# Kernel tuning notes

Hardware: AMD Instinct MI355X
Metric: run time of the kernel (lower is better)

The kernel has to match this reference:

```python
import jax, jax.numpy as jnp
import numpy as np

N_HEAD = 16


def setup_inputs() -> dict:
    key = jax.random.key(0)
    ks = jax.random.split(key, 5)
    B, L, C = 2, 2048, 1024
    s = 0.02
    return {
        "x": jax.random.normal(ks[0], (B, L, C), dtype=jnp.float32),
        "attn_mask": jnp.ones((B, L), dtype=jnp.int64),
        "Wq": jax.random.normal(ks[1], (C, C), dtype=jnp.float32) * s,
        "Wk": jax.random.normal(ks[2], (C, C), dtype=jnp.float32) * s,
        "Wv": jax.random.normal(ks[3], (C, C), dtype=jnp.float32) * s,
        "Wp": jax.random.normal(ks[4], (C, C), dtype=jnp.float32) * s,
    }


def reference(x, attn_mask, Wq, Wk, Wv, Wp):
    B, L, C = x.shape
    H = N_HEAD
    D = C // H
    # nn.Linear(bias=False): y = x @ W.T with W of shape (out, in)
    q = (x @ Wq.T).reshape(B, L, H, D).transpose(0, 2, 1, 3)  # (B,H,L,D)
    k = (x @ Wk.T).reshape(B, L, H, D).transpose(0, 2, 1, 3)
    v = (x @ Wv.T).reshape(B, L, H, D).transpose(0, 2, 1, 3)
    att = jnp.einsum("bhqd,bhkd->bhqk", q, k) / jnp.sqrt(jnp.asarray(D, x.dtype))
    causal = jnp.tril(jnp.ones((L, L), dtype=bool))  # (L,L)
    tok = (attn_mask != 0)[:, None, None, :]  # (B,1,1,L) key-side padding mask
    mask = causal[None, None, :, :] & tok
    att = jnp.where(mask, att, -jnp.inf)
    att = jax.nn.softmax(att, axis=-1)
    # dropout p=0.0 (eval): identity
    y = jnp.einsum("bhqk,bhkd->bhqd", att, v)
    y = y.transpose(0, 2, 1, 3).reshape(B, L, C)
    return y @ Wp.T
```

## Files before the change

### kernel.cpp

```cpp
#include <hip/hip_runtime.h>
#include <hip/hip_bf16.h>
#include <cstdint>

typedef _Float16 f16;
typedef _Float16 f16x4 __attribute__((ext_vector_type(4)));
typedef _Float16 f16x8 __attribute__((ext_vector_type(8)));
typedef float f32x4 __attribute__((ext_vector_type(4)));

#define LNEG (-1e30f)
#define EXP2(x) __builtin_amdgcn_exp2f(x)

__device__ __forceinline__ f32x4 mfma16(f16x8 a, f16x8 b, f32x4 c){
    return __builtin_amdgcn_mfma_f32_16x16x32_f16(a, b, c, 0, 0, 0);
}

__global__ __launch_bounds__(256) void cvt5(
    const float* __restrict__ x,  const float* __restrict__ wq,
    const float* __restrict__ wk, const float* __restrict__ wv,
    const float* __restrict__ wp, f16* __restrict__ dst, int nx4, int nw4)
{
    int i = blockIdx.x * blockDim.x + threadIdx.x;
    const float* src; int off;
    if (i < nx4){ src = x; off = i; }
    else {
        int j = i - nx4;
        int s = j >> 18;
        off = j & (nw4 - 1);
        src = (s == 0) ? wq : (s == 1) ? wk : (s == 2) ? wv : wp;
    }
    float4 v = ((const float4*)src)[off];
    f16x4 o = { (f16)v.x, (f16)v.y, (f16)v.z, (f16)v.w };
    *(f16x4*)&dst[(size_t)i * 4] = o;
}

template<typename OutT>
__global__ __launch_bounds__(256) void gemm_xwt(
    const f16* __restrict__ A, const f16* __restrict__ W0, size_t wstride,
    OutT* __restrict__ out0, size_t ostride, f16* __restrict__ vtout,
    int M, int N, int K)
{
    const int tid  = threadIdx.x;
    const int lane = tid & 63;
    const int w    = tid >> 6;
    const int wr   = w >> 1, wc = w & 1;
    const int m0   = blockIdx.y * 128;
    const int n0   = blockIdx.x * 128;
    const f16* Wz  = W0 + wstride * blockIdx.z;
    OutT* out      = out0 + ostride * blockIdx.z;

    __shared__ f16 At[2][128 * 64];
    __shared__ f16 Bt[2][128 * 64];

    f32x4 acc[4][4] = {};
    f16x8 avr[4], bvr[4];

    int srow[4], scolb[4], sswz[4];
    #pragma unroll
    for (int j = 0; j < 4; ++j){
        int off  = (j * 256 + tid) * 16;
        srow[j]  = off >> 7;
        scolb[j] = off & 127;
        sswz[j]  = srow[j] * 128 + (scolb[j] ^ ((srow[j] & 7) << 4));
    }

    #pragma unroll
    for (int j = 0; j < 4; ++j){
        avr[j] = *(const f16x8*)&A [(size_t)(m0 + srow[j]) * K + (scolb[j] >> 1)];
        bvr[j] = *(const f16x8*)&Wz[(size_t)(n0 + srow[j]) * K + (scolb[j] >> 1)];
    }
    #pragma unroll
    for (int j = 0; j < 4; ++j){
        *(f16x8*)((char*)At[0] + sswz[j]) = avr[j];
        *(f16x8*)((char*)Bt[0] + sswz[j]) = bvr[j];
    }
    __syncthreads();

    const int NT = K >> 6;
    for (int t = 0; t < NT; ++t){
        const int cur = t & 1;
        const bool pre = (t + 1 < NT);
        if (pre){
            const int k0 = (t + 1) << 6;
            #pragma unroll
            for (int j = 0; j < 4; ++j){
                avr[j] = *(const f16x8*)&A [(size_t)(m0 + srow[j]) * K + k0 + (scolb[j] >> 1)];
                bvr[j] = *(const f16x8*)&Wz[(size_t)(n0 + srow[j]) * K + k0 + (scolb[j] >> 1)];
            }
        }
        #pragma unroll
        for (int kk = 0; kk < 2; ++kk){
            f16x8 af[4], bf[4];
            #pragma unroll
            for (int mf = 0; mf < 4; ++mf){
                int row = wr * 64 + mf * 16 + (lane & 15);
                int cb  = (kk * 64 + 16 * (lane >> 4)) ^ ((row & 7) << 4);
                af[mf] = *(const f16x8*)((const char*)At[cur] + row * 128 + cb);
            }
            #pragma unroll
            for (int nf = 0; nf < 4; ++nf){
                int row = wc * 64 + nf * 16 + (lane & 15);
                int cb  = (kk * 64 + 16 * (lane >> 4)) ^ ((row & 7) << 4);
                bf[nf] = *(const f16x8*)((const char*)Bt[cur] + row * 128 + cb);
            }
            #pragma unroll
            for (int mf = 0; mf < 4; ++mf)
                #pragma unroll
                for (int nf = 0; nf < 4; ++nf)
                    acc[mf][nf] = mfma16(af[mf], bf[nf], acc[mf][nf]);
        }
        if (pre){
            const int nb = cur ^ 1;
            #pragma unroll
            for (int j = 0; j < 4; ++j){
                *(f16x8*)((char*)At[nb] + sswz[j]) = avr[j];
                *(f16x8*)((char*)Bt[nb] + sswz[j]) = bvr[j];
            }
        }
        __syncthreads();
    }

    if (vtout != nullptr && blockIdx.z == 2){
        #pragma unroll
        for (int mf = 0; mf < 4; ++mf)
            #pragma unroll
            for (int nf = 0; nf < 4; ++nf){
                int row = m0 + wr * 64 + mf * 16 + 4 * (lane >> 4);
                int col = n0 + wc * 64 + nf * 16 + (lane & 15);
                int bb = row >> 11, ll = row & 2047;
                int bh = bb * 16 + (col >> 6), dd = col & 63;
                f16x4 o = { (f16)acc[mf][nf][0], (f16)acc[mf][nf][1],
                            (f16)acc[mf][nf][2], (f16)acc[mf][nf][3] };
                *(f16x4*)&vtout[((size_t)(bh * 64 + dd)) * 2048 + ll] = o;
            }
    } else {
        #pragma unroll
        for (int mf = 0; mf < 4; ++mf)
            #pragma unroll
            for (int nf = 0; nf < 4; ++nf)
                #pragma unroll
                for (int r = 0; r < 4; ++r){
                    int row = m0 + wr * 64 + mf * 16 + 4 * (lane >> 4) + r;
                    int col = n0 + wc * 64 + nf * 16 + (lane & 15);
                    out[(size_t)row * N + col] = (OutT)acc[mf][nf][r];
                }
    }
}

__global__ __launch_bounds__(256, 4) void attn_fused(
    const f16* __restrict__ q, const f16* __restrict__ k,
    const f16* __restrict__ vt, const int* __restrict__ amask,
    f16* __restrict__ y)
{
    const int tid  = threadIdx.x;
    const int lane = tid & 63;
    const int w    = tid >> 6;
    const int g    = lane >> 4;
    const int qq   = lane & 15;

    const int lin = blockIdx.x;
    const int bh  = ((lin & 7) << 2) | ((lin >> 3) & 3);
    const int qtv = (lin >> 5) & 31;
    const int q5  = (qtv & 7) | ((qtv & 16) >> 1);
    const int qt  = (qtv & 8) ? (31 - q5) : q5;
    const int b = bh >> 4, h = bh & 15;
    const int q0w = qt * 64 + w * 16;
    const int nkt = qt + 1;

    __shared__ char sK[2][64 * 128];
    __shared__ char sV[2][64 * 128];
    __shared__ char sP[4][16 * 128];

    const int srow = (tid * 2) >> 3;
    const int sc8a = (tid * 2) & 7, sc8b = sc8a + 1;
    const int swka = (sc8a * 16) ^ ((srow & 7) << 4);
    const int swkb = (sc8b * 16) ^ ((srow & 7) << 4);
    const f16* kbase  = k  + ((size_t)b * 2048) * 1024 + h * 64;
    const f16* vtbase = vt + (size_t)bh * 64 * 2048;

    const f16 qscale = (f16)(0.125f * 1.44269504088896f);
    f16x8 aq[2];
    #pragma unroll
    for (int f = 0; f < 2; ++f){
        aq[f] = *(const f16x8*)&q[((size_t)(b * 2048 + q0w + qq)) * 1024 + h * 64 + f * 32 + 8 * g];
        #pragma unroll
        for (int j = 0; j < 8; ++j) aq[f][j] *= qscale;
    }

    f32x4 acc_o[4] = {};
    float m_ln = LNEG, l_ln = 0.f;

    char* pbase = sP[w] + qq * 128;
    const int swp = (qq & 7) << 4;

    {
        f16x8 ka  = *(const f16x8*)(kbase  + (size_t)srow * 1024 + sc8a * 8);
        f16x8 kb2 = *(const f16x8*)(kbase  + (size_t)srow * 1024 + sc8b * 8);
        f16x8 va  = *(const f16x8*)(vtbase + (size_t)srow * 2048 + sc8a * 8);
        f16x8 vb  = *(const f16x8*)(vtbase + (size_t)srow * 2048 + sc8b * 8);
        *(f16x8*)(sK[0] + srow * 128 + swka) = ka;
        *(f16x8*)(sK[0] + srow * 128 + swkb) = kb2;
        *(f16x8*)(sV[0] + srow * 128 + swka) = va;
        *(f16x8*)(sV[0] + srow * 128 + swkb) = vb;
    }
    __syncthreads();

    for (int kt = 0; kt < nkt; ++kt){
        const int cur = kt & 1;
        const int k0 = kt * 64;
        const bool pre = (kt + 1 < nkt);

        f16x8 ka, kb2, va, vb;
        if (pre){
            const int nk0 = k0 + 64;
            ka  = *(const f16x8*)(kbase  + (size_t)(nk0 + srow) * 1024 + sc8a * 8);
            kb2 = *(const f16x8*)(kbase  + (size_t)(nk0 + srow) * 1024 + sc8b * 8);
            va  = *(const f16x8*)(vtbase + (size_t)srow * 2048 + nk0 + sc8a * 8);
            vb  = *(const f16x8*)(vtbase + (size_t)srow * 2048 + nk0 + sc8b * 8);
        }

        unsigned long long tokbits = __ballot(amask[b * 2048 + k0 + lane] != 0);
        const bool tokall = (tokbits == ~0ull);

        f32x4 acc_s[4] = {};
        #pragma unroll
        for (int kf = 0; kf < 4; ++kf){
            const int keyl = kf * 16 + qq;
            const char* kr = sK[cur] + keyl * 128;
            const int sw = (keyl & 7) << 4;
            #pragma unroll
            for (int f = 0; f < 2; ++f){
                f16x8 ak = *(const f16x8*)(kr + ((f * 64 + 16 * g) ^ sw));
                acc_s[kf] = mfma16(ak, aq[f], acc_s[kf]);
            }
        }

        const bool fullt = (k0 + 63 <= q0w) && tokall;
        float sv[16];
        #pragma unroll
        for (int kf = 0; kf < 4; ++kf)
            #pragma unroll
            for (int r = 0; r < 4; ++r){
                float s = acc_s[kf][r];
                if (!fullt){
                    const int keyl = kf * 16 + 4 * g + r;
                    const bool ok = (k0 + keyl <= q0w + qq) && ((tokbits >> keyl) & 1);
                    s = ok ? s : LNEG;
                }
                sv[kf * 4 + r] = s;
            }

        float tmax = sv[0];
        #pragma unroll
        for (int i = 1; i < 16; ++i) tmax = fmaxf(tmax, sv[i]);
        tmax = fmaxf(tmax, __shfl_xor(tmax, 16));
        tmax = fmaxf(tmax, __shfl_xor(tmax, 32));
        const bool skip = __all(tmax <= m_ln + 8.f);
        float alpha = 1.f;
        if (!skip){
            const float newm = fmaxf(m_ln, tmax);
            alpha = EXP2(m_ln - newm);
            m_ln = newm;
        }
        float rs = 0.f;
        #pragma unroll
        for (int i = 0; i < 16; ++i){ sv[i] = EXP2(sv[i] - m_ln); rs += sv[i]; }
        rs += __shfl_xor(rs, 16);
        rs += __shfl_xor(rs, 32);
        l_ln = l_ln * alpha + rs;
        if (!skip){
            #pragma unroll
            for (int r = 0; r < 4; ++r){
                const float ar = __shfl(alpha, 4 * g + r);
                #pragma unroll
                for (int nf = 0; nf < 4; ++nf) acc_o[nf][r] *= ar;
            }
        }

        #pragma unroll
        for (int kf = 0; kf < 4; ++kf){
            f16x4 pk = { (f16)sv[kf*4+0], (f16)sv[kf*4+1], (f16)sv[kf*4+2], (f16)sv[kf*4+3] };
            *(f16x4*)(pbase + ((kf * 32 + 8 * g) ^ swp)) = pk;
        }
        __builtin_amdgcn_wave_barrier();

        #pragma unroll
        for (int f = 0; f < 2; ++f){
            f16x8 ap = *(const f16x8*)(pbase + ((f * 64 + 16 * g) ^ swp));
            #pragma unroll
            for (int nf = 0; nf < 4; ++nf){
                const int d = nf * 16 + qq;
                f16x8 bv = *(const f16x8*)(sV[cur] + d * 128 + ((f * 64 + 16 * g) ^ ((d & 7) << 4)));
                acc_o[nf] = mfma16(ap, bv, acc_o[nf]);
            }
        }
        __builtin_amdgcn_wave_barrier();

        if (pre){
            const int nb = cur ^ 1;
            *(f16x8*)(sK[nb] + srow * 128 + swka) = ka;
            *(f16x8*)(sK[nb] + srow * 128 + swkb) = kb2;
            *(f16x8*)(sV[nb] + srow * 128 + swka) = va;
            *(f16x8*)(sV[nb] + srow * 128 + swkb) = vb;
        }
        __syncthreads();
    }

    const float invl = 1.f / l_ln;
    #pragma unroll
    for (int r = 0; r < 4; ++r){
        const float ir = __shfl(invl, 4 * g + r);
        const int row = q0w + 4 * g + r;
        #pragma unroll
        for (int nf = 0; nf < 4; ++nf)
            y[((size_t)(b * 2048 + row)) * 1024 + h * 64 + nf * 16 + qq] = (f16)(acc_o[nf][r] * ir);
    }
}

extern "C" void kernel_launch(void* const* d_in, const int* in_sizes, int n_in,
                              void* d_out, int out_size, void* d_ws, size_t ws_size,
                              hipStream_t stream){
    const float* x  = (const float*)d_in[0];
    const int*   am = (const int*)d_in[1];
    const float* Wq = (const float*)d_in[2];
    const float* Wk = (const float*)d_in[3];
    const float* Wv = (const float*)d_in[4];
    const float* Wp = (const float*)d_in[5];
    float* out = (float*)d_out;

    char* ws = (char*)d_ws;
    const size_t XE = (size_t)4096 * 1024;
    const size_t WE = (size_t)1024 * 1024;

    f16* x16 = (f16*)(ws);
    f16* w16 = (f16*)(ws + XE * 2);
    f16* qkv = (f16*)(ws + XE * 2 + WE * 8);
    f16* vt  = (f16*)(ws + XE * 2 + WE * 8 + XE * 6);
    f16* y16 = (f16*)(ws + XE * 2 + WE * 8 + XE * 8);

    cvt5<<<8192, 256, 0, stream>>>(x, Wq, Wk, Wv, Wp, x16,
                                   (int)(XE / 4), (int)(WE / 4));

    gemm_xwt<f16><<<dim3(8, 32, 3), 256, 0, stream>>>(x16, w16, WE, qkv, XE, vt, 4096, 1024, 1024);

    attn_fused<<<dim3(1024), 256, 0, stream>>>(qkv, qkv + XE, vt, am, y16);

    gemm_xwt<float><<<dim3(8, 32, 1), 256, 0, stream>>>(y16, w16 + 3 * WE, 0, out, 0, nullptr, 4096, 1024, 1024);
}
```

Baseline: 114.1 us.

## Software-pipeline QK^T of next tile with softmax/PV of current tile

Restructures the flash-attention key loop so the QK^T MFMAs for tile kt+1 are issued before the softmax and PV work of tile kt, and global prefetch now runs two tiles ahead. The intent is to overlap matrix-core work with the scalar softmax and LDS traffic, and to hide global-load latency behind more work. In exchange it holds an extra set of score accumulators in registers, which may lower occupancy. It also adds a second block-wide barrier per iteration around the shared-memory refill.

```diff
diff --git a/kernel.cpp b/kernel.cpp
--- a/kernel.cpp
+++ b/kernel.cpp
@@ -204,46 +204,82 @@
     }
     __syncthreads();
 
+    f32x4 accA[4] = {};
+    unsigned long long tok_cur;
+    {
+        const bool has1 = (nkt > 1);
+        f16x8 ka, kb2, va, vb;
+        if (has1){
+            ka  = *(const f16x8*)(kbase  + (size_t)(64 + srow) * 1024 + sc8a * 8);
+            kb2 = *(const f16x8*)(kbase  + (size_t)(64 + srow) * 1024 + sc8b * 8);
+            va  = *(const f16x8*)(vtbase + (size_t)srow * 2048 + 64 + sc8a * 8);
+            vb  = *(const f16x8*)(vtbase + (size_t)srow * 2048 + 64 + sc8b * 8);
+        }
+        const int amv0 = amask[b * 2048 + lane];
+        #pragma unroll
+        for (int kf = 0; kf < 4; ++kf){
+            const int keyl = kf * 16 + qq;
+            const char* kr = sK[0] + keyl * 128;
+            const int sw = (keyl & 7) << 4;
+            #pragma unroll
+            for (int f = 0; f < 2; ++f){
+                f16x8 ak = *(const f16x8*)(kr + ((f * 64 + 16 * g) ^ sw));
+                accA[kf] = mfma16(ak, aq[f], accA[kf]);
+            }
+        }
+        tok_cur = __ballot(amv0 != 0);
+        if (has1){
+            *(f16x8*)(sK[1] + srow * 128 + swka) = ka;
+            *(f16x8*)(sK[1] + srow * 128 + swkb) = kb2;
+            *(f16x8*)(sV[1] + srow * 128 + swka) = va;
+            *(f16x8*)(sV[1] + srow * 128 + swkb) = vb;
+        }
+    }
+    __syncthreads();
+
     for (int kt = 0; kt < nkt; ++kt){
-        const int cur = kt & 1;
+        const int cur = kt & 1, nb = cur ^ 1;
         const int k0 = kt * 64;
-        const bool pre = (kt + 1 < nkt);
+        const bool has1 = (kt + 1 < nkt);
+        const bool has2 = (kt + 2 < nkt);
 
         f16x8 ka, kb2, va, vb;
-        if (pre){
-            const int nk0 = k0 + 64;
+        int amv;
+        if (has2){
+            const int nk0 = k0 + 128;
             ka  = *(const f16x8*)(kbase  + (size_t)(nk0 + srow) * 1024 + sc8a * 8);
             kb2 = *(const f16x8*)(kbase  + (size_t)(nk0 + srow) * 1024 + sc8b * 8);
             va  = *(const f16x8*)(vtbase + (size_t)srow * 2048 + nk0 + sc8a * 8);
             vb  = *(const f16x8*)(vtbase + (size_t)srow * 2048 + nk0 + sc8b * 8);
         }
-
-        unsigned long long tokbits = __ballot(amask[b * 2048 + k0 + lane] != 0);
-        const bool tokall = (tokbits == ~0ull);
-
-        f32x4 acc_s[4] = {};
-        #pragma unroll
-        for (int kf = 0; kf < 4; ++kf){
-            const int keyl = kf * 16 + qq;
-            const char* kr = sK[cur] + keyl * 128;
-            const int sw = (keyl & 7) << 4;
-            #pragma unroll
-            for (int f = 0; f < 2; ++f){
-                f16x8 ak = *(const f16x8*)(kr + ((f * 64 + 16 * g) ^ sw));
-                acc_s[kf] = mfma16(ak, aq[f], acc_s[kf]);
-            }
-        }
-
+        if (has1) amv = amask[b * 2048 + k0 + 64 + lane];
+
+        f32x4 accB[4] = {};
+        if (has1){
+            #pragma unroll
+            for (int kf = 0; kf < 4; ++kf){
+                const int keyl = kf * 16 + qq;
+                const char* kr = sK[nb] + keyl * 128;
+                const int sw = (keyl & 7) << 4;
+                #pragma unroll
+                for (int f = 0; f < 2; ++f){
+                    f16x8 ak = *(const f16x8*)(kr + ((f * 64 + 16 * g) ^ sw));
+                    accB[kf] = mfma16(ak, aq[f], accB[kf]);
+                }
+            }
+        }
+
+        const bool tokall = (tok_cur == ~0ull);
         const bool fullt = (k0 + 63 <= q0w) && tokall;
         float sv[16];
         #pragma unroll
         for (int kf = 0; kf < 4; ++kf)
             #pragma unroll
             for (int r = 0; r < 4; ++r){
-                float s = acc_s[kf][r];
+                float s = accA[kf][r];
                 if (!fullt){
                     const int keyl = kf * 16 + 4 * g + r;
-                    const bool ok = (k0 + keyl <= q0w + qq) && ((tokbits >> keyl) & 1);
+                    const bool ok = (k0 + keyl <= q0w + qq) && ((tok_cur >> keyl) & 1);
                     s = ok ? s : LNEG;
                 }
                 sv[kf * 4 + r] = s;
@@ -293,16 +329,18 @@
                 acc_o[nf] = mfma16(ap, bv, acc_o[nf]);
             }
         }
-        __builtin_amdgcn_wave_barrier();
-
-        if (pre){
-            const int nb = cur ^ 1;
-            *(f16x8*)(sK[nb] + srow * 128 + swka) = ka;
-            *(f16x8*)(sK[nb] + srow * 128 + swkb) = kb2;
-            *(f16x8*)(sV[nb] + srow * 128 + swka) = va;
-            *(f16x8*)(sV[nb] + srow * 128 + swkb) = vb;
-        }
-        __syncthreads();
+
+        if (has2){
+            __syncthreads();
+            *(f16x8*)(sK[cur] + srow * 128 + swka) = ka;
+            *(f16x8*)(sK[cur] + srow * 128 + swkb) = kb2;
+            *(f16x8*)(sV[cur] + srow * 128 + swka) = va;
+            *(f16x8*)(sV[cur] + srow * 128 + swkb) = vb;
+            __syncthreads();
+        }
+        if (has1) tok_cur = __ballot(amv != 0);
+        #pragma unroll
+        for (int i = 0; i < 4; ++i) accA[i] = accB[i];
     }
 
     const float invl = 1.f / l_ln;
```

Result: no change. 115.7 us (+1.5%).
